# Optimization experiments

Hardware: AMD Instinct MI355X
Metric: run time of the kernel (lower is better)

Reference implementation:

```python
import jax, jax.numpy as jnp
import numpy as np

B, C, H, W = 8, 256, 64, 64
OUT, K = 256, 3
OG = 1
STRIDE, PAD, DIL = 1, 1, 1
K2 = K * K


def setup_inputs() -> dict:
    key = jax.random.key(0)
    ks = jax.random.split(key, 5)
    x = jax.random.normal(ks[0], (B, C, H, W), jnp.float32)
    # main deform-conv weight [out, in//groups, k, k]
    weight = jax.random.normal(ks[1], (OUT, C, K, K), jnp.float32) * (1.0 / np.sqrt(C * K2))
    bias = jax.random.normal(ks[2], (OUT,), jnp.float32) * 0.01
    # param_generator: 3x3 conv -> 3*OG*K*K channels (oh, ow, mask)
    pg_w = jax.random.normal(ks[3], (3 * OG * K2, C, 3, 3), jnp.float32) * 0.01
    pg_b = jax.random.normal(ks[4], (3 * OG * K2,), jnp.float32) * 0.01
    return {"x": x, "weight": weight, "bias": bias, "pg_w": pg_w, "pg_b": pg_b}


def _conv3x3(x, w, b):
    y = jax.lax.conv_general_dilated(
        x, w, (1, 1), [(1, 1), (1, 1)],
        dimension_numbers=("NCHW", "OIHW", "NCHW"))
    return y + b[None, :, None, None]


def _bilinear_gather(img, py, px):
    # img [B,C,H,W]; py,px [B,K2,Ho,Wo] -> [B,C,K2,Ho,Wo]
    # Zero padding outside the image (torchvision deform_conv2d semantics).
    Hh, Ww = img.shape[2], img.shape[3]
    y0 = jnp.floor(py)
    x0 = jnp.floor(px)
    dy = py - y0
    dx = px - x0
    imgf = img.reshape(img.shape[0], img.shape[1], Hh * Ww)
    out = jnp.zeros((img.shape[0], img.shape[1]) + py.shape[1:], img.dtype)
    corners = (
        (0, 0, (1 - dy) * (1 - dx)),
        (0, 1, (1 - dy) * dx),
        (1, 0, dy * (1 - dx)),
        (1, 1, dy * dx),
    )
    for oy, ox, wgt in corners:
        yy = y0 + oy
        xx = x0 + ox
        valid = (yy >= 0) & (yy < Hh) & (xx >= 0) & (xx < Ww)
        yi = jnp.clip(yy, 0, Hh - 1).astype(jnp.int32)
        xi = jnp.clip(xx, 0, Ww - 1).astype(jnp.int32)
        idx = yi * Ww + xi  # [B,K2,Ho,Wo]
        g = jax.vmap(lambda im, ix: jnp.take(im, ix.reshape(-1), axis=1))(imgf, idx)
        g = g.reshape(img.shape[0], img.shape[1], *idx.shape[1:])
        out = out + g * (wgt * valid)[:, None]
    return out


def _deform_conv2d(x, weight, bias, pg_w, pg_b):
    Bn = x.shape[0]
    Hi, Wi = x.shape[2], x.shape[3]
    Ho = (Hi + 2 * PAD - DIL * (K - 1) - 1) // STRIDE + 1
    Wo = (Wi + 2 * PAD - DIL * (K - 1) - 1) // STRIDE + 1
    params = _conv3x3(x, pg_w, pg_b)  # [B, 3*OG*K2, H, W]
    oh, ow, mask = jnp.split(params, 3, axis=1)
    offset = jnp.concatenate([oh, ow], axis=1)  # [B, 2*OG*K2, Ho, Wo]
    mask = jax.nn.sigmoid(mask)                  # [B, OG*K2, Ho, Wo]
    # torchvision layout: channel = ((og*K2 + k)*2 + {y,x})
    off = offset.reshape(Bn, OG, K2, 2, Ho, Wo)
    dy = off[:, :, :, 0].reshape(Bn, K2, Ho, Wo)  # OG == 1
    dx = off[:, :, :, 1].reshape(Bn, K2, Ho, Wo)
    hy = jnp.arange(Ho, dtype=x.dtype) * STRIDE - PAD
    wx = jnp.arange(Wo, dtype=x.dtype) * STRIDE - PAD
    ky, kx = jnp.meshgrid(jnp.arange(K), jnp.arange(K), indexing="ij")
    base_y = hy[None, :, None] + (ky.reshape(-1) * DIL).astype(x.dtype)[:, None, None]  # [K2,Ho,1]
    base_x = wx[None, None, :] + (kx.reshape(-1) * DIL).astype(x.dtype)[:, None, None]  # [K2,1,Wo]
    py = dy + base_y[None]  # [B,K2,Ho,Wo]
    px = dx + base_x[None]
    sampled = _bilinear_gather(x, py, px)          # [B,C,K2,Ho,Wo]
    sampled = sampled * mask[:, None]              # modulation (OG=1)
    out = jnp.einsum("bckhw,ock->bohw", sampled, weight.reshape(OUT, C, K2))
    return out + bias[None, :, None, None]


def reference(x, weight, bias, pg_w, pg_b):
    return _deform_conv2d(x, weight, bias, pg_w, pg_b)
```

## Files before the change

### kernel.cpp

```cpp
#include <hip/hip_runtime.h>
#include <math.h>

#define BQ   8
#define CIN  256
#define HH   64
#define WW   64
#define COUT 256
#define K2   9
#define PCH  27

#define PT     64
#define CCH    32
#define NCHUNK (CIN / CCH)
#define KSTEP  9
#define NSTEP  (NCHUNK * KSTEP)
#define SROW   328
#define PLANE  (HH * WW)

typedef __attribute__((ext_vector_type(8))) short short8;
typedef __attribute__((ext_vector_type(4))) float f32x4;
typedef __attribute__((ext_vector_type(2))) float f32x2;

static __device__ __forceinline__ unsigned short f2bf(float f) {
    unsigned u = __builtin_bit_cast(unsigned, f);
    u += 0x7fff + ((u >> 16) & 1);
    return (unsigned short)(u >> 16);
}
static __device__ __forceinline__ f32x2 up2(unsigned u) {
    f32x2 r;
    r[0] = __builtin_bit_cast(float, u << 16);
    r[1] = __builtin_bit_cast(float, u & 0xffff0000u);
    return r;
}
static __device__ __forceinline__ unsigned cvtpk(float lo, float hi) {
    unsigned r;
    asm("v_cvt_pk_bf16_f32 %0, %1, %2" : "=v"(r) : "v"(lo), "v"(hi));
    return r;
}

__global__ __launch_bounds__(256) void k_packw(const float* __restrict__ w,
                                               unsigned short* __restrict__ wp) {
    int t = blockIdx.x * 256 + threadIdx.x;
    if (t >= NSTEP * COUT * 4) return;
    int q = t & 3;
    int o = (t >> 2) & 255;
    int s = t >> 10;
    short8 sv;
#pragma unroll
    for (int j = 0; j < 8; ++j) {
        int pos   = s * 32 + q * 8 + j;
        int chunk = pos / (CCH * K2);
        int pl    = pos % (CCH * K2);
        int ktap  = pl >> 5;
        int c     = chunk * CCH + (pl & 31);
        sv[j] = (short)f2bf(w[(o * CIN + c) * K2 + ktap]);
    }
    *(short8*)(wp + (size_t)t * 8) = sv;
}

__global__ __launch_bounds__(256) void k_packpg(const float* __restrict__ pgw,
                                                unsigned short* __restrict__ wpg) {
    int t = blockIdx.x * 256 + threadIdx.x;
    if (t >= NSTEP * 32 * 4) return;
    int q = t & 3;
    int o = (t >> 2) & 31;
    int s = t >> 7;
    short8 sv;
#pragma unroll
    for (int j = 0; j < 8; ++j) {
        int pos   = s * 32 + q * 8 + j;
        int chunk = pos / (CCH * K2);
        int pl    = pos % (CCH * K2);
        int ktap  = pl >> 5;
        int c     = chunk * CCH + (pl & 31);
        sv[j] = (o < PCH) ? (short)f2bf(pgw[(size_t)(o * CIN + c) * K2 + ktap]) : (short)0;
    }
    *(short8*)(wpg + (size_t)t * 8) = sv;
}

__global__ __launch_bounds__(256) void k_xt(const float* __restrict__ x,
                                            unsigned short* __restrict__ xT) {
    __shared__ float tile[64][65];
    int blk = blockIdx.x;
    int cc  = blk & 3;
    int y   = (blk >> 2) & 63;
    int b   = blk >> 8;
    int t   = threadIdx.x;
    int c0  = cc * 64;

    const float* xp = x + ((size_t)(b * CIN + c0) * HH + y) * WW;
#pragma unroll
    for (int r = 0; r < 16; ++r) {
        int cl = r * 4 + (t >> 6);
        int xx = t & 63;
        tile[cl][xx] = xp[(size_t)cl * PLANE + xx];
    }
    __syncthreads();
    unsigned short* op = xT + ((size_t)b * PLANE + (size_t)y * WW) * CIN + c0;
#pragma unroll
    for (int r = 0; r < 16; ++r) {
        int xx = r * 4 + (t >> 6);
        int cl = t & 63;
        op[(size_t)xx * CIN + cl] = f2bf(tile[cl][xx]);
    }
}

__global__ __launch_bounds__(512, 2) void k_fused(const unsigned short* __restrict__ xT,
                                                  const unsigned short* __restrict__ wp,
                                                  const unsigned short* __restrict__ wpg,
                                                  const float* __restrict__ bias,
                                                  const float* __restrict__ pgb,
                                                  float* __restrict__ out) {
    __shared__ alignas(16) unsigned short s_samp[2][PT][SROW];
    __shared__ float4 s_wgt4[K2][PT];
    __shared__ int4   s_off4[K2][PT];
    __shared__ float  s_params[32][65];

    int blk = blockIdx.x;
    int b   = blk >> 6;
    int h   = blk & 63;
    int t   = threadIdx.x;

    int gp = t >> 3;
    int cg = t & 7;
    int wv = t >> 6;
    int lm = t & 15;
    int lq = (t >> 4) & 3;

    const char* xTb = (const char*)xT + (size_t)b * PLANE * CIN * 2;

    {
        int ipg = wv >> 2;
        int rpg = wv & 3;
        f32x4 accA = (f32x4){0.f, 0.f, 0.f, 0.f};
        f32x4 accB = (f32x4){0.f, 0.f, 0.f, 0.f};

        int  pixo[K2];
        bool okk[K2];
#pragma unroll
        for (int k = 0; k < K2; ++k) {
            int row = h + (k / 3) - 1;
            int col = gp + (k % 3) - 1;
            okk[k]  = ((unsigned)row < (unsigned)HH) & ((unsigned)col < (unsigned)WW);
            int pix = min(max(row, 0), HH - 1) * WW + min(max(col, 0), WW - 1);
            pixo[k] = pix * (CIN * 2) + cg * 8;
        }

        uint2 Ga[K2];
#pragma unroll
        for (int k = 0; k < K2; ++k)
            Ga[k] = *(const uint2*)(xTb + pixo[k]);
#pragma unroll
        for (int k = 0; k < K2; ++k) {
            uint2 d = Ga[k];
            if (!okk[k]) { d.x = 0; d.y = 0; }
            *(uint2*)&s_samp[0][gp][k * CCH + cg * 4] = d;
        }
#pragma unroll
        for (int k = 0; k < K2; ++k)
            Ga[k] = *(const uint2*)(xTb + pixo[k] + (CCH * 2));
        asm volatile("s_waitcnt lgkmcnt(0)" ::: "memory");
        __builtin_amdgcn_s_barrier();

        for (int ch = 0; ch < NCHUNK; ++ch) {
            bool doC = (ch + 1 < NCHUNK);
            bool doL = (ch + 2 < NCHUNK);
            unsigned short (*__restrict__ bc)[SROW] = s_samp[ch & 1];
            unsigned short (*__restrict__ bn)[SROW] = s_samp[(ch + 1) & 1];
            const unsigned short* wb = wpg + (size_t)(ch * KSTEP) * 32 * 32;
            short8 ac = *(const short8*)(wb + (ipg * 16 + lm) * 32 + lq * 8);
#pragma unroll
            for (int sl = 0; sl < KSTEP; ++sl) {
                short8 bf = *(const short8*)&bc[rpg * 16 + lm][sl * 32 + lq * 8];
                short8 an = ac;
                if (sl + 1 < KSTEP)
                    an = *(const short8*)(wb + (size_t)(sl + 1) * 32 * 32
                                          + (ipg * 16 + lm) * 32 + lq * 8);
                if (doC) {
                    uint2 d = Ga[sl];
                    if (!okk[sl]) { d.x = 0; d.y = 0; }
                    *(uint2*)&bn[gp][sl * CCH + cg * 4] = d;
                }
                if (doL)
                    Ga[sl] = *(const uint2*)(xTb + pixo[sl] + (ch + 2) * (CCH * 2));
                if (sl & 1)
                    accB = __builtin_amdgcn_mfma_f32_16x16x32_bf16(ac, bf, accB, 0, 0, 0);
                else
                    accA = __builtin_amdgcn_mfma_f32_16x16x32_bf16(ac, bf, accA, 0, 0, 0);
                ac = an;
            }
            asm volatile("s_waitcnt lgkmcnt(0)" ::: "memory");
            __builtin_amdgcn_s_barrier();
        }
        f32x4 accpg = accA + accB;
#pragma unroll
        for (int rg = 0; rg < 4; ++rg) {
            int oc = ipg * 16 + lq * 4 + rg;
            float bb = (oc < PCH) ? pgb[oc] : 0.f;
            s_params[oc][rpg * 16 + lm] = accpg[rg] + bb;
        }
    }
    __syncthreads();

    for (int e = t; e < K2 * PT; e += 512) {
        int k = e >> 6;
        int p = e & 63;
        float dy = s_params[2 * k][p];
        float dx = s_params[2 * k + 1][p];
        float mz = s_params[18 + k][p];
        float m  = 1.f / (1.f + expf(-mz));

        float py = dy + (float)(h - 1 + k / 3);
        float px = dx + (float)(p - 1 + k % 3);
        float y0f = floorf(py), x0f = floorf(px);
        float fy = py - y0f,    fx = px - x0f;
        int iy0 = (int)y0f, ix0 = (int)x0f;
        int iy1 = iy0 + 1,  ix1 = ix0 + 1;
        bool vy0 = (unsigned)iy0 < (unsigned)HH;
        bool vy1 = (unsigned)iy1 < (unsigned)HH;
        bool vx0 = (unsigned)ix0 < (unsigned)WW;
        bool vx1 = (unsigned)ix1 < (unsigned)WW;

        float w00 = (1.f - fy) * (1.f - fx) * m; if (!(vy0 && vx0)) w00 = 0.f;
        float w01 = (1.f - fy) * fx         * m; if (!(vy0 && vx1)) w01 = 0.f;
        float w10 = fy         * (1.f - fx) * m; if (!(vy1 && vx0)) w10 = 0.f;
        float w11 = fy         * fx         * m; if (!(vy1 && vx1)) w11 = 0.f;

        int cy0 = min(max(iy0, 0), HH - 1), cy1 = min(max(iy1, 0), HH - 1);
        int cx0 = min(max(ix0, 0), WW - 1), cx1 = min(max(ix1, 0), WW - 1);

        s_wgt4[k][p] = make_float4(w00, w01, w10, w11);
        s_off4[k][p] = make_int4((cy0 * WW + cx0) * 512, (cy0 * WW + cx1) * 512,
                                 (cy1 * WW + cx0) * 512, (cy1 * WW + cx1) * 512);
    }
    __syncthreads();

    int ow = wv * 32;
    f32x4 acc[2][4];
#pragma unroll
    for (int i = 0; i < 2; ++i)
#pragma unroll
        for (int j = 0; j < 4; ++j) acc[i][j] = (f32x4){0.f, 0.f, 0.f, 0.f};

    uint2 G[K2][4];
    {
        const int c0 = cg * 8;
#pragma unroll
        for (int k = 0; k < K2; ++k) {
            int4 ob = s_off4[k][gp];
            G[k][0] = *(const uint2*)(xTb + ob.x + c0);
            G[k][1] = *(const uint2*)(xTb + ob.y + c0);
            G[k][2] = *(const uint2*)(xTb + ob.z + c0);
            G[k][3] = *(const uint2*)(xTb + ob.w + c0);
        }
#pragma unroll
        for (int k = 0; k < K2; ++k) {
            float4 gw = s_wgt4[k][gp];
            f32x2 v01 = gw.x * up2(G[k][0].x) + gw.y * up2(G[k][1].x)
                      + gw.z * up2(G[k][2].x) + gw.w * up2(G[k][3].x);
            f32x2 v23 = gw.x * up2(G[k][0].y) + gw.y * up2(G[k][1].y)
                      + gw.z * up2(G[k][2].y) + gw.w * up2(G[k][3].y);
            uint2 pk;
            pk.x = cvtpk(v01[0], v01[1]);
            pk.y = cvtpk(v23[0], v23[1]);
            *(uint2*)&s_samp[0][gp][k * CCH + cg * 4] = pk;
        }
        const int c1 = (CCH * 2) + cg * 8;
#pragma unroll
        for (int k = 0; k < K2; ++k) {
            int4 ob = s_off4[k][gp];
            G[k][0] = *(const uint2*)(xTb + ob.x + c1);
            G[k][1] = *(const uint2*)(xTb + ob.y + c1);
            G[k][2] = *(const uint2*)(xTb + ob.z + c1);
            G[k][3] = *(const uint2*)(xTb + ob.w + c1);
        }
        asm volatile("s_waitcnt lgkmcnt(0)" ::: "memory");
        __builtin_amdgcn_s_barrier();
    }

    for (int ch = 0; ch < NCHUNK; ++ch) {
        bool doC = (ch + 1 < NCHUNK);
        bool doL = (ch + 2 < NCHUNK);
        const int cofl = (ch + 2) * (CCH * 2) + cg * 8;
        unsigned short (*__restrict__ bc)[SROW] = s_samp[ch & 1];
        unsigned short (*__restrict__ bn)[SROW] = s_samp[(ch + 1) & 1];
        const unsigned short* wb = wp + (size_t)(ch * KSTEP) * COUT * 32;
        short8 a0c = *(const short8*)(wb + (ow +  0 + lm) * 32 + lq * 8);
        short8 a1c = *(const short8*)(wb + (ow + 16 + lm) * 32 + lq * 8);
#pragma unroll
        for (int sl = 0; sl < KSTEP; ++sl) {
            short8 b0 = *(const short8*)&bc[ 0 + lm][sl * 32 + lq * 8];
            short8 b1 = *(const short8*)&bc[16 + lm][sl * 32 + lq * 8];
            short8 b2 = *(const short8*)&bc[32 + lm][sl * 32 + lq * 8];
            short8 b3 = *(const short8*)&bc[48 + lm][sl * 32 + lq * 8];
            short8 a0n = a0c, a1n = a1c;
            if (sl + 1 < KSTEP) {
                const unsigned short* wrn = wb + (size_t)(sl + 1) * COUT * 32;
                a0n = *(const short8*)(wrn + (ow +  0 + lm) * 32 + lq * 8);
                a1n = *(const short8*)(wrn + (ow + 16 + lm) * 32 + lq * 8);
            }
            if (doC) {
                float4 gw = s_wgt4[sl][gp];
                f32x2 v01 = gw.x * up2(G[sl][0].x) + gw.y * up2(G[sl][1].x)
                          + gw.z * up2(G[sl][2].x) + gw.w * up2(G[sl][3].x);
                f32x2 v23 = gw.x * up2(G[sl][0].y) + gw.y * up2(G[sl][1].y)
                          + gw.z * up2(G[sl][2].y) + gw.w * up2(G[sl][3].y);
                uint2 pk;
                pk.x = cvtpk(v01[0], v01[1]);
                pk.y = cvtpk(v23[0], v23[1]);
                *(uint2*)&bn[gp][sl * CCH + cg * 4] = pk;
            }
            if (doL) {
                int4 ob = s_off4[sl][gp];
                G[sl][0] = *(const uint2*)(xTb + ob.x + cofl);
                G[sl][1] = *(const uint2*)(xTb + ob.y + cofl);
                G[sl][2] = *(const uint2*)(xTb + ob.z + cofl);
                G[sl][3] = *(const uint2*)(xTb + ob.w + cofl);
            }
            __builtin_amdgcn_s_setprio(1);
            acc[0][0] = __builtin_amdgcn_mfma_f32_16x16x32_bf16(a0c, b0, acc[0][0], 0, 0, 0);
            acc[0][1] = __builtin_amdgcn_mfma_f32_16x16x32_bf16(a0c, b1, acc[0][1], 0, 0, 0);
            acc[0][2] = __builtin_amdgcn_mfma_f32_16x16x32_bf16(a0c, b2, acc[0][2], 0, 0, 0);
            acc[0][3] = __builtin_amdgcn_mfma_f32_16x16x32_bf16(a0c, b3, acc[0][3], 0, 0, 0);
            acc[1][0] = __builtin_amdgcn_mfma_f32_16x16x32_bf16(a1c, b0, acc[1][0], 0, 0, 0);
            acc[1][1] = __builtin_amdgcn_mfma_f32_16x16x32_bf16(a1c, b1, acc[1][1], 0, 0, 0);
            acc[1][2] = __builtin_amdgcn_mfma_f32_16x16x32_bf16(a1c, b2, acc[1][2], 0, 0, 0);
            acc[1][3] = __builtin_amdgcn_mfma_f32_16x16x32_bf16(a1c, b3, acc[1][3], 0, 0, 0);
            __builtin_amdgcn_s_setprio(0);
            a0c = a0n; a1c = a1n;
        }
        asm volatile("s_waitcnt lgkmcnt(0)" ::: "memory");
        __builtin_amdgcn_s_barrier();
    }

    float* ob = out + ((size_t)b * COUT) * PLANE + h * WW;
#pragma unroll
    for (int i = 0; i < 2; ++i) {
        int o0 = ow + i * 16 + lq * 4;
        f32x4 bv = *(const f32x4*)(bias + o0);
#pragma unroll
        for (int rg = 0; rg < 4; ++rg) {
#pragma unroll
            for (int j = 0; j < 4; ++j)
                ob[(size_t)(o0 + rg) * PLANE + j * 16 + lm] = acc[i][j][rg] + bv[rg];
        }
    }
}

extern "C" void kernel_launch(void* const* d_in, const int* in_sizes, int n_in,
                              void* d_out, int out_size, void* d_ws, size_t ws_size,
                              hipStream_t stream) {
    const float* x    = (const float*)d_in[0];
    const float* wgt  = (const float*)d_in[1];
    const float* bias = (const float*)d_in[2];
    const float* pgw  = (const float*)d_in[3];
    const float* pgb  = (const float*)d_in[4];
    float* out = (float*)d_out;

    const size_t WPK_B = (size_t)NSTEP * COUT * 32 * 2;
    const size_t WPG_B = (size_t)NSTEP * 32 * 32 * 2;
    unsigned short* wpk = (unsigned short*)d_ws;
    unsigned short* wpg = (unsigned short*)((char*)d_ws + WPK_B);
    unsigned short* xT  = (unsigned short*)((char*)d_ws + WPK_B + WPG_B);

    k_packw <<<(NSTEP * COUT * 4 + 255) / 256, 256, 0, stream>>>(wgt, wpk);
    k_packpg<<<(NSTEP * 32 * 4 + 255) / 256,   256, 0, stream>>>(pgw, wpg);
    k_xt    <<<BQ * HH * 4, 256, 0, stream>>>(x, xT);
    k_fused <<<BQ * HH, 512, 0, stream>>>(xT, wpk, wpg, bias, pgb, out);
}
```

Before: 125.9 us.

## Split each output row into two half-row blocks with swizzled block mapping

Each workgroup now handles 32 output pixels instead of a full 64-pixel row, which doubles the grid to 1024 blocks and raises launch bounds to 4 blocks per CU. Per-thread gathers narrow from 8 to 4 bytes, with 16 channel groups per pixel. A block-index swizzle spreads the halves and rows across XCDs. The goal is more blocks and higher occupancy to hide gather latency and fill all CUs. In exchange, each block does half the MFMA work per weight fetch, and only half the waves are active in the param-generator GEMM, so weight traffic and per-block overhead roughly double.

After: 148.0 us. 1.17x slower.

```diff
diff --git a/kernel.cpp b/kernel.cpp
--- a/kernel.cpp
+++ b/kernel.cpp
@@ -9,7 +9,7 @@
 #define K2   9
 #define PCH  27
 
-#define PT     64
+#define PT     32
 #define CCH    32
 #define NCHUNK (CIN / CCH)
 #define KSTEP  9
@@ -105,7 +105,7 @@
     }
 }
 
-__global__ __launch_bounds__(512, 2) void k_fused(const unsigned short* __restrict__ xT,
+__global__ __launch_bounds__(512, 4) void k_fused(const unsigned short* __restrict__ xT,
                                                   const unsigned short* __restrict__ wp,
                                                   const unsigned short* __restrict__ wpg,
                                                   const float* __restrict__ bias,
@@ -114,15 +114,18 @@
     __shared__ alignas(16) unsigned short s_samp[2][PT][SROW];
     __shared__ float4 s_wgt4[K2][PT];
     __shared__ int4   s_off4[K2][PT];
-    __shared__ float  s_params[32][65];
+    __shared__ float  s_params[32][33];
 
     int blk = blockIdx.x;
-    int b   = blk >> 6;
-    int h   = blk & 63;
-    int t   = threadIdx.x;
-
-    int gp = t >> 3;
-    int cg = t & 7;
+    int swz = (blk & 7) * 128 + (blk >> 3);
+    int half = swz & 1;
+    int h    = (swz >> 1) & 63;
+    int b    = swz >> 7;
+    int px0  = half * PT;
+    int t    = threadIdx.x;
+
+    int gp = t >> 4;
+    int cg = t & 15;
     int wv = t >> 6;
     int lm = t & 15;
     int lq = (t >> 4) & 3;
@@ -130,8 +133,9 @@
     const char* xTb = (const char*)xT + (size_t)b * PLANE * CIN * 2;
 
     {
-        int ipg = wv >> 2;
-        int rpg = wv & 3;
+        int ipg = wv >> 1;
+        int rpg = wv & 1;
+        bool act = (wv < 4);
         f32x4 accA = (f32x4){0.f, 0.f, 0.f, 0.f};
         f32x4 accB = (f32x4){0.f, 0.f, 0.f, 0.f};
 
@@ -140,27 +144,25 @@
 #pragma unroll
         for (int k = 0; k < K2; ++k) {
             int row = h + (k / 3) - 1;
-            int col = gp + (k % 3) - 1;
+            int col = px0 + gp + (k % 3) - 1;
             okk[k]  = ((unsigned)row < (unsigned)HH) & ((unsigned)col < (unsigned)WW);
             int pix = min(max(row, 0), HH - 1) * WW + min(max(col, 0), WW - 1);
-            pixo[k] = pix * (CIN * 2) + cg * 8;
-        }
-
-        uint2 Ga[K2];
+            pixo[k] = pix * (CIN * 2) + cg * 4;
+        }
+
+        unsigned Ga[K2];
 #pragma unroll
         for (int k = 0; k < K2; ++k)
-            Ga[k] = *(const uint2*)(xTb + pixo[k]);
-#pragma unroll
-        for (int k = 0; k < K2; ++k) {
-            uint2 d = Ga[k];
-            if (!okk[k]) { d.x = 0; d.y = 0; }
-            *(uint2*)&s_samp[0][gp][k * CCH + cg * 4] = d;
+            Ga[k] = *(const unsigned*)(xTb + pixo[k]);
+#pragma unroll
+        for (int k = 0; k < K2; ++k) {
+            unsigned d = okk[k] ? Ga[k] : 0u;
+            *(unsigned*)&s_samp[0][gp][k * CCH + cg * 2] = d;
         }
 #pragma unroll
         for (int k = 0; k < K2; ++k)
-            Ga[k] = *(const uint2*)(xTb + pixo[k] + (CCH * 2));
-        asm volatile("s_waitcnt lgkmcnt(0)" ::: "memory");
-        __builtin_amdgcn_s_barrier();
+            Ga[k] = *(const unsigned*)(xTb + pixo[k] + (CCH * 2));
+        __syncthreads();
 
         for (int ch = 0; ch < NCHUNK; ++ch) {
             bool doC = (ch + 1 < NCHUNK);
@@ -168,50 +170,54 @@
             unsigned short (*__restrict__ bc)[SROW] = s_samp[ch & 1];
             unsigned short (*__restrict__ bn)[SROW] = s_samp[(ch + 1) & 1];
             const unsigned short* wb = wpg + (size_t)(ch * KSTEP) * 32 * 32;
-            short8 ac = *(const short8*)(wb + (ipg * 16 + lm) * 32 + lq * 8);
+            short8 ac = {};
+            if (act) ac = *(const short8*)(wb + (ipg * 16 + lm) * 32 + lq * 8);
 #pragma unroll
             for (int sl = 0; sl < KSTEP; ++sl) {
-                short8 bf = *(const short8*)&bc[rpg * 16 + lm][sl * 32 + lq * 8];
+                short8 bf = {};
+                if (act) bf = *(const short8*)&bc[rpg * 16 + lm][sl * 32 + lq * 8];
                 short8 an = ac;
-                if (sl + 1 < KSTEP)
+                if (act && (sl + 1 < KSTEP))
                     an = *(const short8*)(wb + (size_t)(sl + 1) * 32 * 32
                                           + (ipg * 16 + lm) * 32 + lq * 8);
                 if (doC) {
-                    uint2 d = Ga[sl];
-                    if (!okk[sl]) { d.x = 0; d.y = 0; }
-                    *(uint2*)&bn[gp][sl * CCH + cg * 4] = d;
+                    unsigned d = okk[sl] ? Ga[sl] : 0u;
+                    *(unsigned*)&bn[gp][sl * CCH + cg * 2] = d;
                 }
                 if (doL)
-                    Ga[sl] = *(const uint2*)(xTb + pixo[sl] + (ch + 2) * (CCH * 2));
-                if (sl & 1)
-                    accB = __builtin_amdgcn_mfma_f32_16x16x32_bf16(ac, bf, accB, 0, 0, 0);
-                else
-                    accA = __builtin_amdgcn_mfma_f32_16x16x32_bf16(ac, bf, accA, 0, 0, 0);
+                    Ga[sl] = *(const unsigned*)(xTb + pixo[sl] + (ch + 2) * (CCH * 2));
+                if (act) {
+                    if (sl & 1)
+                        accB = __builtin_amdgcn_mfma_f32_16x16x32_bf16(ac, bf, accB, 0, 0, 0);
+                    else
+                        accA = __builtin_amdgcn_mfma_f32_16x16x32_bf16(ac, bf, accA, 0, 0, 0);
+                }
                 ac = an;
             }
-            asm volatile("s_waitcnt lgkmcnt(0)" ::: "memory");
-            __builtin_amdgcn_s_barrier();
-        }
-        f32x4 accpg = accA + accB;
-#pragma unroll
-        for (int rg = 0; rg < 4; ++rg) {
-            int oc = ipg * 16 + lq * 4 + rg;
-            float bb = (oc < PCH) ? pgb[oc] : 0.f;
-            s_params[oc][rpg * 16 + lm] = accpg[rg] + bb;
+            __syncthreads();
+        }
+        if (act) {
+            f32x4 accpg = accA + accB;
+#pragma unroll
+            for (int rg = 0; rg < 4; ++rg) {
+                int oc = ipg * 16 + lq * 4 + rg;
+                float bb = (oc < PCH) ? pgb[oc] : 0.f;
+                s_params[oc][rpg * 16 + lm] = accpg[rg] + bb;
+            }
         }
     }
     __syncthreads();
 
-    for (int e = t; e < K2 * PT; e += 512) {
-        int k = e >> 6;
-        int p = e & 63;
+    if (t < K2 * PT) {
+        int k = t >> 5;
+        int p = t & 31;
         float dy = s_params[2 * k][p];
         float dx = s_params[2 * k + 1][p];
         float mz = s_params[18 + k][p];
         float m  = 1.f / (1.f + expf(-mz));
 
         float py = dy + (float)(h - 1 + k / 3);
-        float px = dx + (float)(p - 1 + k % 3);
+        float px = dx + (float)(px0 + p - 1 + k % 3);
         float y0f = floorf(py), x0f = floorf(px);
         float fy = py - y0f,    fx = px - x0f;
         int iy0 = (int)y0f, ix0 = (int)x0f;
@@ -236,52 +242,46 @@
     __syncthreads();
 
     int ow = wv * 32;
-    f32x4 acc[2][4];
+    f32x4 acc[2][2];
 #pragma unroll
     for (int i = 0; i < 2; ++i)
 #pragma unroll
-        for (int j = 0; j < 4; ++j) acc[i][j] = (f32x4){0.f, 0.f, 0.f, 0.f};
-
-    uint2 G[K2][4];
+        for (int j = 0; j < 2; ++j) acc[i][j] = (f32x4){0.f, 0.f, 0.f, 0.f};
+
+    unsigned G[K2][4];
     {
-        const int c0 = cg * 8;
+        const int c0 = cg * 4;
 #pragma unroll
         for (int k = 0; k < K2; ++k) {
             int4 ob = s_off4[k][gp];
-            G[k][0] = *(const uint2*)(xTb + ob.x + c0);
-            G[k][1] = *(const uint2*)(xTb + ob.y + c0);
-            G[k][2] = *(const uint2*)(xTb + ob.z + c0);
-            G[k][3] = *(const uint2*)(xTb + ob.w + c0);
+            G[k][0] = *(const unsigned*)(xTb + ob.x + c0);
+            G[k][1] = *(const unsigned*)(xTb + ob.y + c0);
+            G[k][2] = *(const unsigned*)(xTb + ob.z + c0);
+            G[k][3] = *(const unsigned*)(xTb + ob.w + c0);
         }
 #pragma unroll
         for (int k = 0; k < K2; ++k) {
             float4 gw = s_wgt4[k][gp];
-            f32x2 v01 = gw.x * up2(G[k][0].x) + gw.y * up2(G[k][1].x)
-                      + gw.z * up2(G[k][2].x) + gw.w * up2(G[k][3].x);
-            f32x2 v23 = gw.x * up2(G[k][0].y) + gw.y * up2(G[k][1].y)
-                      + gw.z * up2(G[k][2].y) + gw.w * up2(G[k][3].y);
-            uint2 pk;
-            pk.x = cvtpk(v01[0], v01[1]);
-            pk.y = cvtpk(v23[0], v23[1]);
-            *(uint2*)&s_samp[0][gp][k * CCH + cg * 4] = pk;
-        }
-        const int c1 = (CCH * 2) + cg * 8;
+            f32x2 v = gw.x * up2(G[k][0]) + gw.y * up2(G[k][1])
+                    + gw.z * up2(G[k][2]) + gw.w * up2(G[k][3]);
+            *(unsigned*)&s_samp[0][gp][k * CCH + cg * 2] = cvtpk(v[0], v[1]);
+        }
+        const int c1 = (CCH * 2) + cg * 4;
 #pragma unroll
         for (int k = 0; k < K2; ++k) {
             int4 ob = s_off4[k][gp];
-            G[k][0] = *(const uint2*)(xTb + ob.x + c1);
-            G[k][1] = *(const uint2*)(xTb + ob.y + c1);
-            G[k][2] = *(const uint2*)(xTb + ob.z + c1);
-            G[k][3] = *(const uint2*)(xTb + ob.w + c1);
-        }
-        asm volatile("s_waitcnt lgkmcnt(0)" ::: "memory");
-        __builtin_amdgcn_s_barrier();
+            G[k][0] = *(const unsigned*)(xTb + ob.x + c1);
+            G[k][1] = *(const unsigned*)(xTb + ob.y + c1);
+            G[k][2] = *(const unsigned*)(xTb + ob.z + c1);
+            G[k][3] = *(const unsigned*)(xTb + ob.w + c1);
+        }
+        __syncthreads();
     }
 
     for (int ch = 0; ch < NCHUNK; ++ch) {
         bool doC = (ch + 1 < NCHUNK);
         bool doL = (ch + 2 < NCHUNK);
-        const int cofl = (ch + 2) * (CCH * 2) + cg * 8;
+        const int cofl = (ch + 2) * (CCH * 2) + cg * 4;
         unsigned short (*__restrict__ bc)[SROW] = s_samp[ch & 1];
         unsigned short (*__restrict__ bn)[SROW] = s_samp[(ch + 1) & 1];
         const unsigned short* wb = wp + (size_t)(ch * KSTEP) * COUT * 32;
@@ -291,8 +291,6 @@
         for (int sl = 0; sl < KSTEP; ++sl) {
             short8 b0 = *(const short8*)&bc[ 0 + lm][sl * 32 + lq * 8];
             short8 b1 = *(const short8*)&bc[16 + lm][sl * 32 + lq * 8];
-            short8 b2 = *(const short8*)&bc[32 + lm][sl * 32 + lq * 8];
-            short8 b3 = *(const short8*)&bc[48 + lm][sl * 32 + lq * 8];
             short8 a0n = a0c, a1n = a1c;
             if (sl + 1 < KSTEP) {
                 const unsigned short* wrn = wb + (size_t)(sl + 1) * COUT * 32;
@@ -301,39 +299,29 @@
             }
             if (doC) {
                 float4 gw = s_wgt4[sl][gp];
-                f32x2 v01 = gw.x * up2(G[sl][0].x) + gw.y * up2(G[sl][1].x)
-                          + gw.z * up2(G[sl][2].x) + gw.w * up2(G[sl][3].x);
-                f32x2 v23 = gw.x * up2(G[sl][0].y) + gw.y * up2(G[sl][1].y)
-                          + gw.z * up2(G[sl][2].y) + gw.w * up2(G[sl][3].y);
-                uint2 pk;
-                pk.x = cvtpk(v01[0], v01[1]);
-                pk.y = cvtpk(v23[0], v23[1]);
-                *(uint2*)&bn[gp][sl * CCH + cg * 4] = pk;
+                f32x2 v = gw.x * up2(G[sl][0]) + gw.y * up2(G[sl][1])
+                        + gw.z * up2(G[sl][2]) + gw.w * up2(G[sl][3]);
+                *(unsigned*)&bn[gp][sl * CCH + cg * 2] = cvtpk(v[0], v[1]);
             }
             if (doL) {
                 int4 ob = s_off4[sl][gp];
-                G[sl][0] = *(const uint2*)(xTb + ob.x + cofl);
-                G[sl][1] = *(const uint2*)(xTb + ob.y + cofl);
-                G[sl][2] = *(const uint2*)(xTb + ob.z + cofl);
-                G[sl][3] = *(const uint2*)(xTb + ob.w + cofl);
+                G[sl][0] = *(const unsigned*)(xTb + ob.x + cofl);
+                G[sl][1] = *(const unsigned*)(xTb + ob.y + cofl);
+                G[sl][2] = *(const unsigned*)(xTb + ob.z + cofl);
+                G[sl][3] = *(const unsigned*)(xTb + ob.w + cofl);
             }
             __builtin_amdgcn_s_setprio(1);
             acc[0][0] = __builtin_amdgcn_mfma_f32_16x16x32_bf16(a0c, b0, acc[0][0], 0, 0, 0);
             acc[0][1] = __builtin_amdgcn_mfma_f32_16x16x32_bf16(a0c, b1, acc[0][1], 0, 0, 0);
-            acc[0][2] = __builtin_amdgcn_mfma_f32_16x16x32_bf16(a0c, b2, acc[0][2], 0, 0, 0);
-            acc[0][3] = __builtin_amdgcn_mfma_f32_16x16x32_bf16(a0c, b3, acc[0][3], 0, 0, 0);
             acc[1][0] = __builtin_amdgcn_mfma_f32_16x16x32_bf16(a1c, b0, acc[1][0], 0, 0, 0);
             acc[1][1] = __builtin_amdgcn_mfma_f32_16x16x32_bf16(a1c, b1, acc[1][1], 0, 0, 0);
-            acc[1][2] = __builtin_amdgcn_mfma_f32_16x16x32_bf16(a1c, b2, acc[1][2], 0, 0, 0);
-            acc[1][3] = __builtin_amdgcn_mfma_f32_16x16x32_bf16(a1c, b3, acc[1][3], 0, 0, 0);
             __builtin_amdgcn_s_setprio(0);
             a0c = a0n; a1c = a1n;
         }
-        asm volatile("s_waitcnt lgkmcnt(0)" ::: "memory");
-        __builtin_amdgcn_s_barrier();
-    }
-
-    float* ob = out + ((size_t)b * COUT) * PLANE + h * WW;
+        __syncthreads();
+    }
+
+    float* op = out + ((size_t)b * COUT) * PLANE + h * WW + px0;
 #pragma unroll
     for (int i = 0; i < 2; ++i) {
         int o0 = ow + i * 16 + lq * 4;
@@ -341,8 +329,8 @@
 #pragma unroll
         for (int rg = 0; rg < 4; ++rg) {
 #pragma unroll
-            for (int j = 0; j < 4; ++j)
-                ob[(size_t)(o0 + rg) * PLANE + j * 16 + lm] = acc[i][j][rg] + bv[rg];
+            for (int j = 0; j < 2; ++j)
+                op[(size_t)(o0 + rg) * PLANE + j * 16 + lm] = acc[i][j][rg] + bv[rg];
         }
     }
 }
@@ -366,5 +354,5 @@
     k_packw <<<(NSTEP * COUT * 4 + 255) / 256, 256, 0, stream>>>(wgt, wpk);
     k_packpg<<<(NSTEP * 32 * 4 + 255) / 256,   256, 0, stream>>>(pgw, wpg);
     k_xt    <<<BQ * HH * 4, 256, 0, stream>>>(x, xT);
-    k_fused <<<BQ * HH, 512, 0, stream>>>(xT, wpk, wpg, bias, pgb, out);
-}
+    k_fused <<<BQ * HH * 2, 512, 0, stream>>>(xT, wpk, wpg, bias, pgb, out);
+}
```

## Shrink pipeline stages to three taps to cut LDS and registers, raise occupancy

Applied to the files above, without the earlier changes.

Splits each 32-channel chunk's nine kernel taps into three sub-stages of three taps. The double-buffered sample tile shrinks from 9 taps to 3 taps per row, and the in-flight gather registers drop from 9×4 to 3×4. Launch bounds go from 2 to 4 blocks per CU to exploit the lower LDS and VGPR footprint. Block indices are also swizzled across batches. The cost is three times as many barriers per chunk and shorter stages, which leave less room to hide gather latency behind MFMA work.

Result: faster. 120.2 us (-4.6%).

```diff
diff --git a/kernel.cpp b/kernel.cpp
--- a/kernel.cpp
+++ b/kernel.cpp
@@ -12,14 +12,20 @@
 #define PT     64
 #define CCH    32
 #define NCHUNK (CIN / CCH)
-#define KSTEP  9
-#define NSTEP  (NCHUNK * KSTEP)
-#define SROW   328
+#define NSTEP  72
+#define NSUB   24
+#define SUBROW 104
 #define PLANE  (HH * WW)
 
 typedef __attribute__((ext_vector_type(8))) short short8;
 typedef __attribute__((ext_vector_type(4))) float f32x4;
 typedef __attribute__((ext_vector_type(2))) float f32x2;
+
+#define PIPE_BARRIER() do {                                   \
+    asm volatile("s_waitcnt lgkmcnt(0)" ::: "memory");        \
+    __builtin_amdgcn_s_barrier();                             \
+    asm volatile("" ::: "memory");                            \
+} while (0)
 
 static __device__ __forceinline__ unsigned short f2bf(float f) {
     unsigned u = __builtin_bit_cast(unsigned, f);
@@ -105,20 +111,21 @@
     }
 }
 
-__global__ __launch_bounds__(512, 2) void k_fused(const unsigned short* __restrict__ xT,
+__global__ __launch_bounds__(512, 4) void k_fused(const unsigned short* __restrict__ xT,
                                                   const unsigned short* __restrict__ wp,
                                                   const unsigned short* __restrict__ wpg,
                                                   const float* __restrict__ bias,
                                                   const float* __restrict__ pgb,
                                                   float* __restrict__ out) {
-    __shared__ alignas(16) unsigned short s_samp[2][PT][SROW];
+    __shared__ alignas(16) unsigned short s_samp[2][PT][SUBROW];
     __shared__ float4 s_wgt4[K2][PT];
     __shared__ int4   s_off4[K2][PT];
     __shared__ float  s_params[32][65];
 
     int blk = blockIdx.x;
-    int b   = blk >> 6;
-    int h   = blk & 63;
+    int swz = (blk & 7) * 64 + (blk >> 3);
+    int b   = swz >> 6;
+    int h   = swz & 63;
     int t   = threadIdx.x;
 
     int gp = t >> 3;
@@ -146,51 +153,52 @@
             pixo[k] = pix * (CIN * 2) + cg * 8;
         }
 
-        uint2 Ga[K2];
-#pragma unroll
-        for (int k = 0; k < K2; ++k)
-            Ga[k] = *(const uint2*)(xTb + pixo[k]);
-#pragma unroll
-        for (int k = 0; k < K2; ++k) {
-            uint2 d = Ga[k];
-            if (!okk[k]) { d.x = 0; d.y = 0; }
-            *(uint2*)&s_samp[0][gp][k * CCH + cg * 4] = d;
-        }
-#pragma unroll
-        for (int k = 0; k < K2; ++k)
-            Ga[k] = *(const uint2*)(xTb + pixo[k] + (CCH * 2));
-        asm volatile("s_waitcnt lgkmcnt(0)" ::: "memory");
-        __builtin_amdgcn_s_barrier();
-
-        for (int ch = 0; ch < NCHUNK; ++ch) {
-            bool doC = (ch + 1 < NCHUNK);
-            bool doL = (ch + 2 < NCHUNK);
-            unsigned short (*__restrict__ bc)[SROW] = s_samp[ch & 1];
-            unsigned short (*__restrict__ bn)[SROW] = s_samp[(ch + 1) & 1];
-            const unsigned short* wb = wpg + (size_t)(ch * KSTEP) * 32 * 32;
-            short8 ac = *(const short8*)(wb + (ipg * 16 + lm) * 32 + lq * 8);
-#pragma unroll
-            for (int sl = 0; sl < KSTEP; ++sl) {
+        uint2 Ga[3];
+#pragma unroll
+        for (int j = 0; j < 3; ++j)
+            Ga[j] = *(const uint2*)(xTb + pixo[j]);
+#pragma unroll
+        for (int j = 0; j < 3; ++j) {
+            uint2 d = Ga[j];
+            if (!okk[j]) { d.x = 0; d.y = 0; }
+            *(uint2*)&s_samp[0][gp][j * 32 + cg * 4] = d;
+        }
+#pragma unroll
+        for (int j = 0; j < 3; ++j)
+            Ga[j] = *(const uint2*)(xTb + pixo[3 + j]);
+        PIPE_BARRIER();
+
+        short8 ac = *(const short8*)(wpg + (ipg * 16 + lm) * 32 + lq * 8);
+        for (int sc = 0; sc < NSUB; ++sc) {
+            bool doC = (sc + 1 < NSUB);
+            bool doL = (sc + 2 < NSUB);
+            int t1 = ((sc + 1) % 3) * 3;
+            int t2 = ((sc + 2) % 3) * 3;
+            int c2 = ((sc + 2) / 3) * (CCH * 2);
+            unsigned short (*__restrict__ bc)[SUBROW] = s_samp[sc & 1];
+            unsigned short (*__restrict__ bn)[SUBROW] = s_samp[(sc + 1) & 1];
+#pragma unroll
+            for (int sl = 0; sl < 3; ++sl) {
                 short8 bf = *(const short8*)&bc[rpg * 16 + lm][sl * 32 + lq * 8];
+                int r = sc * 3 + sl + 1;
                 short8 an = ac;
-                if (sl + 1 < KSTEP)
-                    an = *(const short8*)(wb + (size_t)(sl + 1) * 32 * 32
+                if (r < NSTEP)
+                    an = *(const short8*)(wpg + (size_t)r * 32 * 32
                                           + (ipg * 16 + lm) * 32 + lq * 8);
                 if (doC) {
                     uint2 d = Ga[sl];
-                    if (!okk[sl]) { d.x = 0; d.y = 0; }
-                    *(uint2*)&bn[gp][sl * CCH + cg * 4] = d;
+                    if (!okk[t1 + sl]) { d.x = 0; d.y = 0; }
+                    *(uint2*)&bn[gp][sl * 32 + cg * 4] = d;
                 }
                 if (doL)
-                    Ga[sl] = *(const uint2*)(xTb + pixo[sl] + (ch + 2) * (CCH * 2));
+                    Ga[sl] = *(const uint2*)(xTb + pixo[t2 + sl] + c2);
                 if (sl & 1)
                     accB = __builtin_amdgcn_mfma_f32_16x16x32_bf16(ac, bf, accB, 0, 0, 0);
                 else
                     accA = __builtin_amdgcn_mfma_f32_16x16x32_bf16(ac, bf, accA, 0, 0, 0);
                 ac = an;
             }
-            asm volatile("s_waitcnt lgkmcnt(0)" ::: "memory");
-            __builtin_amdgcn_s_barrier();
+            PIPE_BARRIER();
         }
         f32x4 accpg = accA + accB;
 #pragma unroll
@@ -242,65 +250,64 @@
 #pragma unroll
         for (int j = 0; j < 4; ++j) acc[i][j] = (f32x4){0.f, 0.f, 0.f, 0.f};
 
-    uint2 G[K2][4];
+    uint2 G[3][4];
     {
-        const int c0 = cg * 8;
-#pragma unroll
-        for (int k = 0; k < K2; ++k) {
-            int4 ob = s_off4[k][gp];
-            G[k][0] = *(const uint2*)(xTb + ob.x + c0);
-            G[k][1] = *(const uint2*)(xTb + ob.y + c0);
-            G[k][2] = *(const uint2*)(xTb + ob.z + c0);
-            G[k][3] = *(const uint2*)(xTb + ob.w + c0);
-        }
-#pragma unroll
-        for (int k = 0; k < K2; ++k) {
-            float4 gw = s_wgt4[k][gp];
-            f32x2 v01 = gw.x * up2(G[k][0].x) + gw.y * up2(G[k][1].x)
-                      + gw.z * up2(G[k][2].x) + gw.w * up2(G[k][3].x);
-            f32x2 v23 = gw.x * up2(G[k][0].y) + gw.y * up2(G[k][1].y)
-                      + gw.z * up2(G[k][2].y) + gw.w * up2(G[k][3].y);
+#pragma unroll
+        for (int j = 0; j < 3; ++j) {
+            int4 ob = s_off4[j][gp];
+            G[j][0] = *(const uint2*)(xTb + ob.x + cg * 8);
+            G[j][1] = *(const uint2*)(xTb + ob.y + cg * 8);
+            G[j][2] = *(const uint2*)(xTb + ob.z + cg * 8);
+            G[j][3] = *(const uint2*)(xTb + ob.w + cg * 8);
+        }
+#pragma unroll
+        for (int j = 0; j < 3; ++j) {
+            float4 gw = s_wgt4[j][gp];
+            f32x2 v01 = gw.x * up2(G[j][0].x) + gw.y * up2(G[j][1].x)
+                      + gw.z * up2(G[j][2].x) + gw.w * up2(G[j][3].x);
+            f32x2 v23 = gw.x * up2(G[j][0].y) + gw.y * up2(G[j][1].y)
+                      + gw.z * up2(G[j][2].y) + gw.w * up2(G[j][3].y);
             uint2 pk;
             pk.x = cvtpk(v01[0], v01[1]);
             pk.y = cvtpk(v23[0], v23[1]);
-            *(uint2*)&s_samp[0][gp][k * CCH + cg * 4] = pk;
-        }
-        const int c1 = (CCH * 2) + cg * 8;
-#pragma unroll
-        for (int k = 0; k < K2; ++k) {
-            int4 ob = s_off4[k][gp];
-            G[k][0] = *(const uint2*)(xTb + ob.x + c1);
-            G[k][1] = *(const uint2*)(xTb + ob.y + c1);
-            G[k][2] = *(const uint2*)(xTb + ob.z + c1);
-            G[k][3] = *(const uint2*)(xTb + ob.w + c1);
-        }
-        asm volatile("s_waitcnt lgkmcnt(0)" ::: "memory");
-        __builtin_amdgcn_s_barrier();
-    }
-
-    for (int ch = 0; ch < NCHUNK; ++ch) {
-        bool doC = (ch + 1 < NCHUNK);
-        bool doL = (ch + 2 < NCHUNK);
-        const int cofl = (ch + 2) * (CCH * 2) + cg * 8;
-        unsigned short (*__restrict__ bc)[SROW] = s_samp[ch & 1];
-        unsigned short (*__restrict__ bn)[SROW] = s_samp[(ch + 1) & 1];
-        const unsigned short* wb = wp + (size_t)(ch * KSTEP) * COUT * 32;
-        short8 a0c = *(const short8*)(wb + (ow +  0 + lm) * 32 + lq * 8);
-        short8 a1c = *(const short8*)(wb + (ow + 16 + lm) * 32 + lq * 8);
-#pragma unroll
-        for (int sl = 0; sl < KSTEP; ++sl) {
+            *(uint2*)&s_samp[0][gp][j * 32 + cg * 4] = pk;
+        }
+#pragma unroll
+        for (int j = 0; j < 3; ++j) {
+            int4 ob = s_off4[3 + j][gp];
+            G[j][0] = *(const uint2*)(xTb + ob.x + cg * 8);
+            G[j][1] = *(const uint2*)(xTb + ob.y + cg * 8);
+            G[j][2] = *(const uint2*)(xTb + ob.z + cg * 8);
+            G[j][3] = *(const uint2*)(xTb + ob.w + cg * 8);
+        }
+        PIPE_BARRIER();
+    }
+
+    short8 a0c = *(const short8*)(wp + (ow +  0 + lm) * 32 + lq * 8);
+    short8 a1c = *(const short8*)(wp + (ow + 16 + lm) * 32 + lq * 8);
+    for (int sc = 0; sc < NSUB; ++sc) {
+        bool doC = (sc + 1 < NSUB);
+        bool doL = (sc + 2 < NSUB);
+        int t1 = ((sc + 1) % 3) * 3;
+        int t2 = ((sc + 2) % 3) * 3;
+        int c2 = ((sc + 2) / 3) * (CCH * 2) + cg * 8;
+        unsigned short (*__restrict__ bc)[SUBROW] = s_samp[sc & 1];
+        unsigned short (*__restrict__ bn)[SUBROW] = s_samp[(sc + 1) & 1];
+#pragma unroll
+        for (int sl = 0; sl < 3; ++sl) {
             short8 b0 = *(const short8*)&bc[ 0 + lm][sl * 32 + lq * 8];
             short8 b1 = *(const short8*)&bc[16 + lm][sl * 32 + lq * 8];
             short8 b2 = *(const short8*)&bc[32 + lm][sl * 32 + lq * 8];
             short8 b3 = *(const short8*)&bc[48 + lm][sl * 32 + lq * 8];
+            int r = sc * 3 + sl + 1;
             short8 a0n = a0c, a1n = a1c;
-            if (sl + 1 < KSTEP) {
-                const unsigned short* wrn = wb + (size_t)(sl + 1) * COUT * 32;
+            if (r < NSTEP) {
+                const unsigned short* wrn = wp + (size_t)r * COUT * 32;
                 a0n = *(const short8*)(wrn + (ow +  0 + lm) * 32 + lq * 8);
                 a1n = *(const short8*)(wrn + (ow + 16 + lm) * 32 + lq * 8);
             }
             if (doC) {
-                float4 gw = s_wgt4[sl][gp];
+                float4 gw = s_wgt4[t1 + sl][gp];
                 f32x2 v01 = gw.x * up2(G[sl][0].x) + gw.y * up2(G[sl][1].x)
                           + gw.z * up2(G[sl][2].x) + gw.w * up2(G[sl][3].x);
                 f32x2 v23 = gw.x * up2(G[sl][0].y) + gw.y * up2(G[sl][1].y)
@@ -308,14 +315,14 @@
                 uint2 pk;
                 pk.x = cvtpk(v01[0], v01[1]);
                 pk.y = cvtpk(v23[0], v23[1]);
-                *(uint2*)&bn[gp][sl * CCH + cg * 4] = pk;
+                *(uint2*)&bn[gp][sl * 32 + cg * 4] = pk;
             }
             if (doL) {
-                int4 ob = s_off4[sl][gp];
-                G[sl][0] = *(const uint2*)(xTb + ob.x + cofl);
-                G[sl][1] = *(const uint2*)(xTb + ob.y + cofl);
-                G[sl][2] = *(const uint2*)(xTb + ob.z + cofl);
-                G[sl][3] = *(const uint2*)(xTb + ob.w + cofl);
+                int4 ob = s_off4[t2 + sl][gp];
+                G[sl][0] = *(const uint2*)(xTb + ob.x + c2);
+                G[sl][1] = *(const uint2*)(xTb + ob.y + c2);
+                G[sl][2] = *(const uint2*)(xTb + ob.z + c2);
+                G[sl][3] = *(const uint2*)(xTb + ob.w + c2);
             }
             __builtin_amdgcn_s_setprio(1);
             acc[0][0] = __builtin_amdgcn_mfma_f32_16x16x32_bf16(a0c, b0, acc[0][0], 0, 0, 0);
@@ -329,11 +336,10 @@
             __builtin_amdgcn_s_setprio(0);
             a0c = a0n; a1c = a1n;
         }
-        asm volatile("s_waitcnt lgkmcnt(0)" ::: "memory");
-        __builtin_amdgcn_s_barrier();
-    }
-
-    float* ob = out + ((size_t)b * COUT) * PLANE + h * WW;
+        PIPE_BARRIER();
+    }
+
+    float* op = out + ((size_t)b * COUT) * PLANE + h * WW;
 #pragma unroll
     for (int i = 0; i < 2; ++i) {
         int o0 = ow + i * 16 + lq * 4;
@@ -342,7 +348,7 @@
         for (int rg = 0; rg < 4; ++rg) {
 #pragma unroll
             for (int j = 0; j < 4; ++j)
-                ob[(size_t)(o0 + rg) * PLANE + j * 16 + lm] = acc[i][j][rg] + bv[rg];
+                op[(size_t)(o0 + rg) * PLANE + j * 16 + lm] = acc[i][j][rg] + bv[rg];
         }
     }
 }
```
